# Performance work log

Measured on AMD Instinct MI355X. Metric: run time of the kernel, lower is better.

Reference implementation:

```python
import jax, jax.numpy as jnp
import numpy as np

TGT, SRC, BATCH, HID, ATT = 64, 64, 32, 512, 512

def setup_inputs() -> dict:
    key = jax.random.key(0)
    k1, k2, k3, k4 = jax.random.split(key, 4)
    h_t = jax.random.normal(k1, (TGT, BATCH, HID), dtype=jnp.float32)
    src_encodings = jax.random.normal(k2, (SRC, BATCH, HID), dtype=jnp.float32)
    # Wa: Linear(2*HID -> ATT, bias=False); stored as (in, out) for jnp.
    Wa = jax.random.normal(k3, (2 * HID, ATT), dtype=jnp.float32) * (1.0 / np.sqrt(2 * HID))
    # Va: Linear(ATT -> 1, bias=False)
    Va = jax.random.normal(k4, (ATT,), dtype=jnp.float32) * (1.0 / np.sqrt(ATT))
    return {"h_t": h_t, "src_encodings": src_encodings, "Wa": Wa, "Va": Va}

def reference(h_t, src_encodings, Wa, Va):
    # Wa([h_t, src]) = h_t @ Wa_h + src @ Wa_s (exact by linearity of concat-matmul)
    Wa_h, Wa_s = Wa[:HID], Wa[HID:]                 # (H, A) each
    h_part = jnp.einsum('tbh,ha->tba', h_t, Wa_h)   # (T, B, A)
    s_part = jnp.einsum('sbh,ha->sba', src_encodings, Wa_s)  # (S, B, A)
    # scores[s, t, b] = Va . tanh(h_part[t,b] + s_part[s,b])
    hidden = jnp.tanh(h_part[None, :, :, :] + s_part[:, None, :, :])  # (S, T, B, A)
    scores = jnp.einsum('stba,a->stb', hidden, Va)  # (S, T, B)
    attn = jax.nn.softmax(scores, axis=0)           # softmax over src dim
    # context[t,b,:] = sum_s attn[s,t,b] * src[s,b,:]
    context = jnp.einsum('stb,sbh->tbh', attn, src_encodings)  # (T, B, H)
    return context
```

## Files before the change

### kernel.cpp

```cpp
#include <hip/hip_runtime.h>
#include <hip/hip_bf16.h>

#define TGT   64
#define SRCN  64
#define BATCH 32
#define HID   512
#define ATT   512
#define MROWS (TGT * BATCH)

typedef __bf16 bf16_t;
typedef __bf16 bf16x8 __attribute__((ext_vector_type(8)));
typedef float  f32x4  __attribute__((ext_vector_type(4)));

__device__ __forceinline__ float fast_exp2(float x) {
#if __has_builtin(__builtin_amdgcn_exp2f)
  return __builtin_amdgcn_exp2f(x);
#else
  float r; asm("v_exp_f32 %0, %1\n\ts_nop 1" : "=v"(r) : "v"(x)); return r;
#endif
}
__device__ __forceinline__ float fast_rcp(float x) {
#if __has_builtin(__builtin_amdgcn_rcpf)
  return __builtin_amdgcn_rcpf(x);
#else
  float r; asm("v_rcp_f32 %0, %1\n\ts_nop 1" : "=v"(r) : "v"(x)); return r;
#endif
}

#define MFMA(a, b, c) __builtin_amdgcn_mfma_f32_16x16x32_bf16((a), (b), (c), 0, 0, 0)

__device__ __forceinline__ unsigned short bfbits(float f) {
  bf16_t h = (bf16_t)f;
  return __builtin_bit_cast(unsigned short, h);
}

__global__ __launch_bounds__(512) void proj_gemm(
    const float* __restrict__ h_t, const float* __restrict__ srcp,
    const float* __restrict__ Wa, float* __restrict__ C)
{
  const int z = blockIdx.z;
  const float* __restrict__ A = z ? srcp : h_t;
  const int mbase = blockIdx.x * 64;
  const int nbase = blockIdx.y * 128;

  __shared__ bf16_t Ah[64][72];
  __shared__ bf16_t Al[64][72];
  __shared__ bf16_t Bh[128][72];
  __shared__ bf16_t Bl[128][72];

  const int tid  = threadIdx.x;
  const int lane = tid & 63;
  const int wv   = tid >> 6;
  const int wm   = (wv & 1) * 32;
  const int wn   = (wv >> 1) * 32;
  const int l15  = lane & 15;
  const int qd   = lane >> 4;

  const int arow = tid >> 3;
  const int akc  = (tid & 7) * 8;
  const int kp = tid >> 4;
  const int nb = tid & 15;

  const float* Aptr = A + (size_t)(mbase + arow) * HID + akc;
  const float* Bptr = Wa + (size_t)(z * HID + 2 * kp) * ATT + nbase + nb;

  f32x4 acc00 = {0.f, 0.f, 0.f, 0.f};
  f32x4 acc01 = acc00, acc10 = acc00, acc11 = acc00;

  for (int kb = 0; kb < HID; kb += 64) {
    if (kb) __syncthreads();

    {
      float4 a0 = *(const float4*)(Aptr + kb);
      float4 a1 = *(const float4*)(Aptr + kb + 4);
      float av[8] = {a0.x, a0.y, a0.z, a0.w, a1.x, a1.y, a1.z, a1.w};
      bf16x8 hi, lo;
#pragma unroll
      for (int j = 0; j < 8; ++j) {
        bf16_t h = (bf16_t)av[j];
        hi[j] = h;
        lo[j] = (bf16_t)(av[j] - (float)h);
      }
      *(bf16x8*)&Ah[arow][akc] = hi;
      *(bf16x8*)&Al[arow][akc] = lo;
    }

    {
      const float* bp = Bptr + (size_t)kb * ATT;
#pragma unroll
      for (int j = 0; j < 8; ++j) {
        float w0 = bp[16 * j];
        float w1 = bp[ATT + 16 * j];
        bf16_t h0 = (bf16_t)w0, h1 = (bf16_t)w1;
        float lo0 = w0 - (float)h0, lo1 = w1 - (float)h1;
        unsigned int uh = (unsigned int)__builtin_bit_cast(unsigned short, h0) |
                          ((unsigned int)__builtin_bit_cast(unsigned short, h1) << 16);
        unsigned int ul = (unsigned int)bfbits(lo0) | ((unsigned int)bfbits(lo1) << 16);
        *(unsigned int*)&Bh[nb + 16 * j][2 * kp] = uh;
        *(unsigned int*)&Bl[nb + 16 * j][2 * kp] = ul;
      }
    }
    __syncthreads();

#pragma unroll
    for (int h = 0; h < 2; ++h) {
      const int kh = h * 32 + qd * 8;
      bf16x8 ah0 = *(const bf16x8*)&Ah[wm + l15][kh];
      bf16x8 ah1 = *(const bf16x8*)&Ah[wm + 16 + l15][kh];
      bf16x8 al0 = *(const bf16x8*)&Al[wm + l15][kh];
      bf16x8 al1 = *(const bf16x8*)&Al[wm + 16 + l15][kh];
      bf16x8 bh0 = *(const bf16x8*)&Bh[wn + l15][kh];
      bf16x8 bh1 = *(const bf16x8*)&Bh[wn + 16 + l15][kh];
      bf16x8 bl0 = *(const bf16x8*)&Bl[wn + l15][kh];
      bf16x8 bl1 = *(const bf16x8*)&Bl[wn + 16 + l15][kh];

      acc00 = MFMA(ah0, bh0, acc00);
      acc01 = MFMA(ah0, bh1, acc01);
      acc10 = MFMA(ah1, bh0, acc10);
      acc11 = MFMA(ah1, bh1, acc11);
      acc00 = MFMA(al0, bh0, acc00);
      acc01 = MFMA(al0, bh1, acc01);
      acc10 = MFMA(al1, bh0, acc10);
      acc11 = MFMA(al1, bh1, acc11);
      acc00 = MFMA(ah0, bl0, acc00);
      acc01 = MFMA(ah0, bl1, acc01);
      acc10 = MFMA(ah1, bl0, acc10);
      acc11 = MFMA(ah1, bl1, acc11);
    }
  }

  float* Cz = C + (size_t)z * (MROWS * ATT);
#pragma unroll
  for (int r = 0; r < 4; ++r) {
    int row0 = mbase + wm + qd * 4 + r;
    int row1 = row0 + 16;
    int col0 = nbase + wn + l15;
    Cz[(size_t)row0 * ATT + col0]      = acc00[r];
    Cz[(size_t)row0 * ATT + col0 + 16] = acc01[r];
    Cz[(size_t)row1 * ATT + col0]      = acc10[r];
    Cz[(size_t)row1 * ATT + col0 + 16] = acc11[r];
  }
}

__global__ __launch_bounds__(512) void attn_fused(
    const float* __restrict__ ws, const float* __restrict__ srcp,
    const float* __restrict__ Va, float* __restrict__ out)
{
  const float* __restrict__ h_part = ws;
  const float* __restrict__ s_part = ws + (size_t)TGT * BATCH * ATT;
  const float SC = 2.8853900817779268f;

  const int t0   = blockIdx.x * 4;
  const int b    = blockIdx.y;
  const int tid  = threadIdx.x;
  const int lane = tid & 63;
  const int wv   = tid >> 6;

  __shared__ float scoreLds[4][64];
  __shared__ float attnLds[4][64];

  const int abase = lane * 8;
  float va[8], H[4][8];
  *(float4*)&va[0] = *(const float4*)(Va + abase);
  *(float4*)&va[4] = *(const float4*)(Va + abase + 4);

  float vsum = 0.f;
#pragma unroll
  for (int j = 0; j < 8; ++j) vsum += va[j];
#pragma unroll
  for (int off = 32; off; off >>= 1) vsum += __shfl_xor(vsum, off);

#pragma unroll
  for (int t = 0; t < 4; ++t) {
    const float* hp = h_part + ((size_t)(t0 + t) * BATCH + b) * ATT + abase;
    float4 h0 = *(const float4*)hp;
    float4 h1 = *(const float4*)(hp + 4);
    H[t][0] = h0.x * SC; H[t][1] = h0.y * SC; H[t][2] = h0.z * SC; H[t][3] = h0.w * SC;
    H[t][4] = h1.x * SC; H[t][5] = h1.y * SC; H[t][6] = h1.z * SC; H[t][7] = h1.w * SC;
  }

#pragma unroll 2
  for (int i = 0; i < 8; ++i) {
    const int s = wv * 8 + i;
    const float* sp = s_part + ((size_t)s * BATCH + b) * ATT + abase;
    float4 s0 = *(const float4*)sp;
    float4 s1 = *(const float4*)(sp + 4);
    float sv[8] = {s0.x * SC, s0.y * SC, s0.z * SC, s0.w * SC,
                   s1.x * SC, s1.y * SC, s1.z * SC, s1.w * SC};
    float q0 = 0.f, q1 = 0.f, q2 = 0.f, q3 = 0.f;
#pragma unroll
    for (int j = 0; j < 8; ++j) {
      float xv = sv[j];
      float vj = va[j];
      q0 = fmaf(vj, fast_rcp(fast_exp2(xv + H[0][j]) + 1.0f), q0);
      q1 = fmaf(vj, fast_rcp(fast_exp2(xv + H[1][j]) + 1.0f), q1);
      q2 = fmaf(vj, fast_rcp(fast_exp2(xv + H[2][j]) + 1.0f), q2);
      q3 = fmaf(vj, fast_rcp(fast_exp2(xv + H[3][j]) + 1.0f), q3);
    }
#pragma unroll
    for (int off = 32; off; off >>= 1) {
      q0 += __shfl_xor(q0, off);
      q1 += __shfl_xor(q1, off);
      q2 += __shfl_xor(q2, off);
      q3 += __shfl_xor(q3, off);
    }
    if (lane == 0) {
      scoreLds[0][s] = vsum - 2.0f * q0;
      scoreLds[1][s] = vsum - 2.0f * q1;
      scoreLds[2][s] = vsum - 2.0f * q2;
      scoreLds[3][s] = vsum - 2.0f * q3;
    }
  }
  __syncthreads();

  if (wv < 4) {
    float sc = scoreLds[wv][lane];
    float m = sc;
#pragma unroll
    for (int off = 32; off; off >>= 1) m = fmaxf(m, __shfl_xor(m, off));
    float e = fast_exp2((sc - m) * 1.4426950408889634f);
    float ssum = e;
#pragma unroll
    for (int off = 32; off; off >>= 1) ssum += __shfl_xor(ssum, off);
    attnLds[wv][lane] = e * fast_rcp(ssum);
  }
  __syncthreads();

  {
    float c0 = 0.f, c1 = 0.f, c2 = 0.f, c3 = 0.f;
    const float* sb = srcp + (size_t)b * HID + tid;
#pragma unroll 8
    for (int s = 0; s < SRCN; ++s) {
      float sv = sb[(size_t)s * BATCH * HID];
      c0 = fmaf(attnLds[0][s], sv, c0);
      c1 = fmaf(attnLds[1][s], sv, c1);
      c2 = fmaf(attnLds[2][s], sv, c2);
      c3 = fmaf(attnLds[3][s], sv, c3);
    }
    out[((size_t)(t0 + 0) * BATCH + b) * HID + tid] = c0;
    out[((size_t)(t0 + 1) * BATCH + b) * HID + tid] = c1;
    out[((size_t)(t0 + 2) * BATCH + b) * HID + tid] = c2;
    out[((size_t)(t0 + 3) * BATCH + b) * HID + tid] = c3;
  }
}

extern "C" void kernel_launch(void* const* d_in, const int* in_sizes, int n_in,
                              void* d_out, int out_size, void* d_ws, size_t ws_size,
                              hipStream_t stream) {
  const float* h_t = (const float*)d_in[0];
  const float* src = (const float*)d_in[1];
  const float* Wa  = (const float*)d_in[2];
  const float* Va  = (const float*)d_in[3];
  float* out = (float*)d_out;
  float* C   = (float*)d_ws;

  proj_gemm<<<dim3(32, 4, 2), 512, 0, stream>>>(h_t, src, Wa, C);
  attn_fused<<<dim3(16, 32), 512, 0, stream>>>(C, src, Va, out);
}
```

Measured before the change: 103.6 us.

## Shrink projection GEMM tile to 64x64 with 256 threads and vectorized B staging

The projection GEMM tile width drops from 128 to 64 columns and threads per block from 512 to 256. Twice as many blocks are launched, which should fill more compute units. B staging changes from scattered 32-bit LDS stores to each thread loading 16 K-rows of one column and writing 128-bit bf16x8 vectors. Each block loads less B and each thread does more conversion work, and the A tile is now re-read by twice as many column blocks.

```diff
diff --git a/kernel.cpp b/kernel.cpp
--- a/kernel.cpp
+++ b/kernel.cpp
@@ -29,24 +29,19 @@
 
 #define MFMA(a, b, c) __builtin_amdgcn_mfma_f32_16x16x32_bf16((a), (b), (c), 0, 0, 0)
 
-__device__ __forceinline__ unsigned short bfbits(float f) {
-  bf16_t h = (bf16_t)f;
-  return __builtin_bit_cast(unsigned short, h);
-}
-
-__global__ __launch_bounds__(512) void proj_gemm(
+__global__ __launch_bounds__(256) void proj_gemm(
     const float* __restrict__ h_t, const float* __restrict__ srcp,
     const float* __restrict__ Wa, float* __restrict__ C)
 {
   const int z = blockIdx.z;
   const float* __restrict__ A = z ? srcp : h_t;
   const int mbase = blockIdx.x * 64;
-  const int nbase = blockIdx.y * 128;
+  const int nbase = blockIdx.y * 64;
 
   __shared__ bf16_t Ah[64][72];
   __shared__ bf16_t Al[64][72];
-  __shared__ bf16_t Bh[128][72];
-  __shared__ bf16_t Bl[128][72];
+  __shared__ bf16_t Bh[64][72];
+  __shared__ bf16_t Bl[64][72];
 
   const int tid  = threadIdx.x;
   const int lane = tid & 63;
@@ -56,13 +51,13 @@
   const int l15  = lane & 15;
   const int qd   = lane >> 4;
 
-  const int arow = tid >> 3;
-  const int akc  = (tid & 7) * 8;
-  const int kp = tid >> 4;
-  const int nb = tid & 15;
+  const int arow = tid >> 2;
+  const int akc  = (tid & 3) * 16;
+  const int bn = tid & 63;
+  const int bkg = (tid >> 6) * 16;
 
   const float* Aptr = A + (size_t)(mbase + arow) * HID + akc;
-  const float* Bptr = Wa + (size_t)(z * HID + 2 * kp) * ATT + nbase + nb;
+  const float* Bptr = Wa + (size_t)(z * HID + bkg) * ATT + nbase + bn;
 
   f32x4 acc00 = {0.f, 0.f, 0.f, 0.f};
   f32x4 acc01 = acc00, acc10 = acc00, acc11 = acc00;
@@ -73,32 +68,45 @@
     {
       float4 a0 = *(const float4*)(Aptr + kb);
       float4 a1 = *(const float4*)(Aptr + kb + 4);
-      float av[8] = {a0.x, a0.y, a0.z, a0.w, a1.x, a1.y, a1.z, a1.w};
-      bf16x8 hi, lo;
+      float4 a2 = *(const float4*)(Aptr + kb + 8);
+      float4 a3 = *(const float4*)(Aptr + kb + 12);
+      float av[16] = {a0.x, a0.y, a0.z, a0.w, a1.x, a1.y, a1.z, a1.w,
+                      a2.x, a2.y, a2.z, a2.w, a3.x, a3.y, a3.z, a3.w};
+      bf16x8 hi0, hi1, lo0, lo1;
 #pragma unroll
       for (int j = 0; j < 8; ++j) {
         bf16_t h = (bf16_t)av[j];
-        hi[j] = h;
-        lo[j] = (bf16_t)(av[j] - (float)h);
+        hi0[j] = h;
+        lo0[j] = (bf16_t)(av[j] - (float)h);
+        bf16_t h2 = (bf16_t)av[j + 8];
+        hi1[j] = h2;
+        lo1[j] = (bf16_t)(av[j + 8] - (float)h2);
       }
-      *(bf16x8*)&Ah[arow][akc] = hi;
-      *(bf16x8*)&Al[arow][akc] = lo;
+      *(bf16x8*)&Ah[arow][akc]     = hi0;
+      *(bf16x8*)&Ah[arow][akc + 8] = hi1;
+      *(bf16x8*)&Al[arow][akc]     = lo0;
+      *(bf16x8*)&Al[arow][akc + 8] = lo1;
     }
 
     {
       const float* bp = Bptr + (size_t)kb * ATT;
+      float bv[16];
+#pragma unroll
+      for (int j = 0; j < 16; ++j) bv[j] = bp[(size_t)j * ATT];
+      bf16x8 hi0, hi1, lo0, lo1;
 #pragma unroll
       for (int j = 0; j < 8; ++j) {
-        float w0 = bp[16 * j];
-        float w1 = bp[ATT + 16 * j];
-        bf16_t h0 = (bf16_t)w0, h1 = (bf16_t)w1;
-        float lo0 = w0 - (float)h0, lo1 = w1 - (float)h1;
-        unsigned int uh = (unsigned int)__builtin_bit_cast(unsigned short, h0) |
-                          ((unsigned int)__builtin_bit_cast(unsigned short, h1) << 16);
-        unsigned int ul = (unsigned int)bfbits(lo0) | ((unsigned int)bfbits(lo1) << 16);
-        *(unsigned int*)&Bh[nb + 16 * j][2 * kp] = uh;
-        *(unsigned int*)&Bl[nb + 16 * j][2 * kp] = ul;
+        bf16_t h = (bf16_t)bv[j];
+        hi0[j] = h;
+        lo0[j] = (bf16_t)(bv[j] - (float)h);
+        bf16_t h2 = (bf16_t)bv[j + 8];
+        hi1[j] = h2;
+        lo1[j] = (bf16_t)(bv[j + 8] - (float)h2);
       }
+      *(bf16x8*)&Bh[bn][bkg]     = hi0;
+      *(bf16x8*)&Bh[bn][bkg + 8] = hi1;
+      *(bf16x8*)&Bl[bn][bkg]     = lo0;
+      *(bf16x8*)&Bl[bn][bkg + 8] = lo1;
     }
     __syncthreads();
 
@@ -254,6 +262,6 @@
   float* out = (float*)d_out;
   float* C   = (float*)d_ws;
 
-  proj_gemm<<<dim3(32, 4, 2), 512, 0, stream>>>(h_t, src, Wa, C);
+  proj_gemm<<<dim3(32, 8, 2), 256, 0, stream>>>(h_t, src, Wa, C);
   attn_fused<<<dim3(16, 32), 512, 0, stream>>>(C, src, Va, out);
 }
```

Result: faster. 100.3 us (-3.2%).
